# Kernel optimization log

Measured on AMD Instinct MI355X. Metric: run time of the kernel, lower is better.

The kernel has to match this reference:

```python
import jax, jax.numpy as jnp
import numpy as np

DIM = 128

def _mlp2(x, W1, b1, W2, b2):
    return jax.nn.relu(x @ W1 + b1) @ W2 + b2

def setup_inputs() -> dict:
    key = jax.random.key(0)
    ks = jax.random.split(key, 16)
    n_var, n_con, n_nodes = 600000, 400000, 1000000
    s2 = 1.0 / np.sqrt(2.0)
    sd = 1.0 / np.sqrt(DIM)
    inp = {
        'var_node_features': jax.random.normal(ks[0], (n_var, 2), jnp.float32),
        'con_node_features': jax.random.normal(ks[1], (n_con, 2), jnp.float32),
        'node_types': jnp.zeros((n_nodes,), jnp.int32),
        'assoc_var': jnp.arange(n_var, dtype=jnp.int64),
        'assoc_con': jnp.arange(n_con, dtype=jnp.int64),
        # var_mlp params
        'vW1': jax.random.uniform(ks[2], (2, DIM), jnp.float32, -s2, s2),
        'vb1': jnp.zeros((DIM,), jnp.float32),
        'vW2': jax.random.uniform(ks[3], (DIM, DIM), jnp.float32, -sd, sd),
        'vb2': jnp.zeros((DIM,), jnp.float32),
        # con_mlp params
        'cW1': jax.random.uniform(ks[4], (2, DIM), jnp.float32, -s2, s2),
        'cb1': jnp.zeros((DIM,), jnp.float32),
        'cW2': jax.random.uniform(ks[5], (DIM, DIM), jnp.float32, -sd, sd),
        'cb2': jnp.zeros((DIM,), jnp.float32),
        # head params fc1..fc4
        'W1': jax.random.uniform(ks[6], (DIM, DIM), jnp.float32, -sd, sd),
        'b1': jnp.zeros((DIM,), jnp.float32),
        'W2': jax.random.uniform(ks[7], (DIM, DIM), jnp.float32, -sd, sd),
        'b2': jnp.zeros((DIM,), jnp.float32),
        'W3': jax.random.uniform(ks[8], (DIM, DIM), jnp.float32, -sd, sd),
        'b3': jnp.zeros((DIM,), jnp.float32),
        'W4': jax.random.uniform(ks[9], (DIM, 1), jnp.float32, -sd, sd),
        'b4': jnp.zeros((1,), jnp.float32),
    }
    return inp

def reference(var_node_features, con_node_features, node_types, assoc_var, assoc_con,
              vW1, vb1, vW2, vb2, cW1, cb1, cW2, cb2,
              W1, b1, W2, b2, W3, b3, W4, b4):
    n = _mlp2(var_node_features, vW1, vb1, vW2, vb2)   # [n_var, dim]
    e = _mlp2(con_node_features, cW1, cb1, cW2, cb2)   # [n_con, dim]
    # scatter into shared node tensor (var first, then con overwrites)
    x = jnp.zeros((node_types.shape[0], n.shape[-1]), n.dtype)
    x = x.at[assoc_var].set(n)
    x = x.at[assoc_con].set(e)
    # gather variable-node embeddings
    x = x[assoc_var]                                   # [n_var, dim]
    x = jax.nn.relu(x @ W1 + b1)  # dropout is identity in eval mode
    x = jax.nn.relu(x @ W2 + b2)
    x = jax.nn.relu(x @ W3 + b3)
    x = jax.nn.sigmoid(x @ W4 + b4)
    return x.squeeze(-1)
```

## Files before the change

### kernel.cpp

```cpp
#include <hip/hip_runtime.h>
#include <hip/hip_bf16.h>

typedef unsigned short u16;
typedef unsigned int u32;
typedef __attribute__((ext_vector_type(8))) short short8;
typedef __attribute__((ext_vector_type(4))) float f32x4;
typedef __attribute__((ext_vector_type(4))) u32 u32x4;

#define MFMA16(a, b, c) __builtin_amdgcn_mfma_f32_16x16x32_bf16((a), (b), (c), 0, 0, 0)
#define S8(v) __builtin_bit_cast(short8, (v))
#define SBAR() __builtin_amdgcn_sched_barrier(0)

__device__ __forceinline__ u32 pack2(float a, float b) {
    union { __hip_bfloat162 h; u32 u; } v;
    v.h = __float22bfloat162_rn(make_float2(a, b));
    return v.u;
}
__device__ __forceinline__ u16 f2b(float f) {
    union { float f; u32 i; } v; v.f = f;
    u32 x = v.i;
    return (u16)((x + 0x7FFFu + ((x >> 16) & 1u)) >> 16);
}

__device__ __forceinline__ void gl_lds16(const u16* g, u16* l) {
    __builtin_amdgcn_global_load_lds(
        (const __attribute__((address_space(1))) void*)g,
        (__attribute__((address_space(3))) void*)l, 16, 0, 0);
}

__global__ void wt_prep(const float* __restrict__ vW2, const float* __restrict__ cW2,
                        const float* __restrict__ W1f, const float* __restrict__ W2f,
                        const float* __restrict__ W3f, u16* __restrict__ wt) {
    int i = blockIdx.x * 256 + threadIdx.x;
    if (i >= 5 * 16384) return;
    int l = i >> 14, e = i & 16383;
    int fr = e >> 9, lane = (e >> 3) & 63, j = e & 7;
    int ot = fr >> 2, ks = fr & 3;
    int c = lane & 15, q = lane >> 4;
    int f = 32 * ks + 16 * (j >> 2) + 4 * q + (j & 3);
    const float* src = (l == 0) ? vW2 : (l == 1) ? cW2 : (l == 2) ? W1f
                     : (l == 3) ? W2f : W3f;
    wt[i] = f2b(src[f * 128 + ot * 16 + c]);
}


#define STAGE(LSRC, B) do {                                                   \
    _Pragma("unroll")                                                         \
    for (int r = 0; r < 4; ++r) {                                             \
        int ch = r * 8 + wv;                                                  \
        gl_lds16(WT + (size_t)(LSRC) * 16384 + ch * 512 + lane * 8,           \
                 ldsw + (B) * 16384 + ch * 512);                              \
    } } while (0)

#define LDSH(B, QQ, H) do {                                                   \
    const u16* _lp = ldsw + (B) * 16384 + ((QQ) * 8 + (H) * 2) * 512 + lane * 8; \
    wu0 = *(const short8*)(_lp + 0 * 512);                                    \
    wu1 = *(const short8*)(_lp + 1 * 512);                                    \
    wu2 = *(const short8*)(_lp + 4 * 512);                                    \
    wu3 = *(const short8*)(_lp + 5 * 512);                                    \
} while (0)

#define BIVL(LB, QQ) do {                                                     \
    biv0 = *(const f32x4*)(ldsb + (LB) * 128 + ((QQ) * 2 + 0) * 16 + q * 4);  \
    biv1 = *(const f32x4*)(ldsb + (LB) * 128 + ((QQ) * 2 + 1) * 16 + q * 4);  \
} while (0)

#define HALF0(I) do {                                                         \
    ac00 = MFMA16(wu0, S8(I##_r0_k0), biv0);                                  \
    ac01 = MFMA16(wu0, S8(I##_r1_k0), biv0);                                  \
    ac10 = MFMA16(wu2, S8(I##_r0_k0), biv1);                                  \
    ac11 = MFMA16(wu2, S8(I##_r1_k0), biv1);                                  \
    ac00 = MFMA16(wu1, S8(I##_r0_k1), ac00);                                  \
    ac01 = MFMA16(wu1, S8(I##_r1_k1), ac01);                                  \
    ac10 = MFMA16(wu3, S8(I##_r0_k1), ac10);                                  \
    ac11 = MFMA16(wu3, S8(I##_r1_k1), ac11);                                  \
} while (0)

#define HALF1(I) do {                                                         \
    ac00 = MFMA16(wu0, S8(I##_r0_k2), ac00);                                  \
    ac01 = MFMA16(wu0, S8(I##_r1_k2), ac01);                                  \
    ac10 = MFMA16(wu2, S8(I##_r0_k2), ac10);                                  \
    ac11 = MFMA16(wu2, S8(I##_r1_k2), ac11);                                  \
    ac00 = MFMA16(wu1, S8(I##_r0_k3), ac00);                                  \
    ac01 = MFMA16(wu1, S8(I##_r1_k3), ac01);                                  \
    ac10 = MFMA16(wu3, S8(I##_r0_k3), ac10);                                  \
    ac11 = MFMA16(wu3, S8(I##_r1_k3), ac11);                                  \
} while (0)

#define EPI(RELU, ACC, OUT, C0, C1)                                           \
  { float v0 = ACC[0], v1 = ACC[1], v2 = ACC[2], v3 = ACC[3];                 \
    if (RELU) { v0 = fmaxf(v0, 0.f); v1 = fmaxf(v1, 0.f);                     \
                v2 = fmaxf(v2, 0.f); v3 = fmaxf(v3, 0.f); }                   \
    OUT.C0 = pack2(v0, v1); OUT.C1 = pack2(v2, v3); }

#define QUARTER(B, LB, I, O, QQ, RELU) do {                                   \
    BIVL(LB, QQ);                                                             \
    LDSH(B, QQ, 0);                                                           \
    HALF0(I);                                                                 \
    LDSH(B, QQ, 1);                                                           \
    HALF1(I);                                                                 \
    EPI(RELU, ac00, O##_r0_k##QQ, x, y)                                       \
    EPI(RELU, ac01, O##_r1_k##QQ, x, y)                                       \
    EPI(RELU, ac10, O##_r0_k##QQ, z, w)                                       \
    EPI(RELU, ac11, O##_r1_k##QQ, z, w)                                       \
} while (0)

#define LAYER(B, LB, I, O, RELU)                                              \
    QUARTER(B, LB, I, O, 0, RELU);                                            \
    QUARTER(B, LB, I, O, 1, RELU);                                            \
    QUARTER(B, LB, I, O, 2, RELU);                                            \
    QUARTER(B, LB, I, O, 3, RELU);

#define QUARTER_LAST(B, I, QQ) do {                                           \
    BIVL(3, QQ);                                                              \
    f32x4 ww0 = *(const f32x4*)(ldsb + 512 + ((QQ) * 2 + 0) * 16 + q * 4);    \
    f32x4 ww1 = *(const f32x4*)(ldsb + 512 + ((QQ) * 2 + 1) * 16 + q * 4);    \
    LDSH(B, QQ, 0);                                                           \
    HALF0(I);                                                                 \
    LDSH(B, QQ, 1);                                                           \
    HALF1(I);                                                                 \
    pd0 += fmaxf(ac00[0], 0.f) * ww0[0] + fmaxf(ac00[1], 0.f) * ww0[1]        \
         + fmaxf(ac00[2], 0.f) * ww0[2] + fmaxf(ac00[3], 0.f) * ww0[3];       \
    pd0 += fmaxf(ac10[0], 0.f) * ww1[0] + fmaxf(ac10[1], 0.f) * ww1[1]        \
         + fmaxf(ac10[2], 0.f) * ww1[2] + fmaxf(ac10[3], 0.f) * ww1[3];       \
    pd1 += fmaxf(ac01[0], 0.f) * ww0[0] + fmaxf(ac01[1], 0.f) * ww0[1]        \
         + fmaxf(ac01[2], 0.f) * ww0[2] + fmaxf(ac01[3], 0.f) * ww0[3];       \
    pd1 += fmaxf(ac11[0], 0.f) * ww1[0] + fmaxf(ac11[1], 0.f) * ww1[1]        \
         + fmaxf(ac11[2], 0.f) * ww1[2] + fmaxf(ac11[3], 0.f) * ww1[3];       \
} while (0)

#define P0_ROW(V, C0, C1, I0, I1)                                             \
  { float x0 = fmaxf(fmaf(I0, wA.x, fmaf(I1, wB.x, bz.x)), 0.f);              \
    float x1 = fmaxf(fmaf(I0, wA.y, fmaf(I1, wB.y, bz.y)), 0.f);              \
    float x2 = fmaxf(fmaf(I0, wA.z, fmaf(I1, wB.z, bz.z)), 0.f);              \
    float x3 = fmaxf(fmaf(I0, wA.w, fmaf(I1, wB.w, bz.w)), 0.f);              \
    V.C0 = pack2(x0, x1); V.C1 = pack2(x2, x3); }

#define P0_HI(KS, HI, C0, C1)                                                 \
  { const int base = (KS) * 32 + (HI) * 16 + q * 4;                           \
    float4 wA = *(const float4*)(w1p + base);                                 \
    float4 wB = *(const float4*)(w1p + 128 + base);                           \
    float4 bz = *(const float4*)(b1p + base);                                 \
    P0_ROW(a_r0_k##KS, C0, C1, in00, in10)                                    \
    P0_ROW(a_r1_k##KS, C0, C1, in01, in11) }

#define P0_KS(KS) P0_HI(KS, 0, x, y) P0_HI(KS, 1, z, w)

#define P0_IN(RT, I0, I1)                                                     \
  { int g = rowW + (RT) * 16 + c; I0 = 0.f; I1 = 0.f;                         \
    if (g < limit) { float2 t2 = *(const float2*)(fb + 2 * g); I0 = t2.x; I1 = t2.y; } }

__global__ __attribute__((amdgpu_flat_work_group_size(512, 512),
                          amdgpu_waves_per_eu(4))) void
mlp_fused(
    const float* __restrict__ varf, const float* __restrict__ conf,
    const float* __restrict__ vW1, const float* __restrict__ vb1, const float* __restrict__ vb2,
    const float* __restrict__ cW1, const float* __restrict__ cb1, const float* __restrict__ cb2,
    const float* __restrict__ b1,  const float* __restrict__ b2,  const float* __restrict__ b3,
    const float* __restrict__ W4,  const float* __restrict__ b4,
    const u16* __restrict__ WT,   float* __restrict__ out,
    int n_var, int n_con, int nb_con)
{
    const int t = threadIdx.x;
    const int lane = t & 63, wv = t >> 6;
    const int c = lane & 15, q = lane >> 4;
    const int bid = blockIdx.x;
    const bool use_con = (bid < nb_con);
    const int row0 = use_con ? bid * 256 : n_con + (bid - nb_con) * 256;
    const int rowW = row0 + wv * 32;
    const int limit = use_con ? n_con : n_var;

    __shared__ u16 ldsw[2 * 16384];
    __shared__ float ldsb[640];

    u32x4 a_r0_k0, a_r0_k1, a_r0_k2, a_r0_k3;
    u32x4 a_r1_k0, a_r1_k1, a_r1_k2, a_r1_k3;
    u32x4 b_r0_k0, b_r0_k1, b_r0_k2, b_r0_k3;
    u32x4 b_r1_k0, b_r1_k1, b_r1_k2, b_r1_k3;
    short8 wu0, wu1, wu2, wu3;
    f32x4 biv0, biv1;
    f32x4 ac00, ac01, ac10, ac11;

    const float* bs0 = use_con ? cb2 : vb2;

    STAGE((use_con ? 1 : 0), 0);
    STAGE(2, 1);
    {
        int which = t >> 7, idx = t & 127;
        const float* p = (which == 0) ? bs0 : (which == 1) ? b1
                       : (which == 2) ? b2 : b3;
        ldsb[t >= 512 ? 0 : t] = (t >= 512) ? ldsb[0] : p[idx];
        if (t < 128) ldsb[512 + t] = W4[t];
    }
    SBAR();

    {
        const float* w1p = use_con ? cW1 : vW1;
        const float* b1p = use_con ? cb1 : vb1;
        const float* fb  = use_con ? conf : varf;
        float in00, in01, in10, in11;
        P0_IN(0, in00, in10) P0_IN(1, in01, in11)
        P0_KS(0) P0_KS(1) P0_KS(2) P0_KS(3)
    }

    float pd0 = 0.f, pd1 = 0.f;

    __syncthreads();

    LAYER(0, 0, a, b, 0)
    __syncthreads();
    STAGE(3, 0);  SBAR();

    LAYER(1, 1, b, a, 1)
    __syncthreads();
    STAGE(4, 1);  SBAR();

    LAYER(0, 2, a, b, 1)
    __syncthreads();

    QUARTER_LAST(1, b, 0);
    QUARTER_LAST(1, b, 1);
    QUARTER_LAST(1, b, 2);
    QUARTER_LAST(1, b, 3);

    float bias4 = b4[0];
#define REDUCE(PD, RT)                                                        \
    { float v = PD;                                                           \
      v += __shfl_xor(v, 16);                                                 \
      v += __shfl_xor(v, 32);                                                 \
      if (q == 0) {                                                           \
          int g = rowW + (RT) * 16 + c;                                       \
          if (g < limit) out[g] = 1.f / (1.f + __expf(-(v + bias4)));         \
      } }
    REDUCE(pd0, 0) REDUCE(pd1, 1)
#undef REDUCE
}

extern "C" void kernel_launch(void* const* d_in, const int* in_sizes, int n_in,
                              void* d_out, int out_size, void* d_ws, size_t ws_size,
                              hipStream_t stream) {
    const float* varf = (const float*)d_in[0];
    const float* conf = (const float*)d_in[1];
    const float* vW1 = (const float*)d_in[5];
    const float* vb1 = (const float*)d_in[6];
    const float* vW2 = (const float*)d_in[7];
    const float* vb2 = (const float*)d_in[8];
    const float* cW1 = (const float*)d_in[9];
    const float* cb1 = (const float*)d_in[10];
    const float* cW2 = (const float*)d_in[11];
    const float* cb2 = (const float*)d_in[12];
    const float* W1  = (const float*)d_in[13];
    const float* b1  = (const float*)d_in[14];
    const float* W2  = (const float*)d_in[15];
    const float* b2  = (const float*)d_in[16];
    const float* W3  = (const float*)d_in[17];
    const float* b3  = (const float*)d_in[18];
    const float* W4  = (const float*)d_in[19];
    const float* b4  = (const float*)d_in[20];

    int n_var = in_sizes[0] / 2;
    int n_con = in_sizes[1] / 2;
    u16* wt = (u16*)d_ws;

    hipLaunchKernelGGL(wt_prep, dim3(320), dim3(256), 0, stream,
                       vW2, cW2, W1, W2, W3, wt);

    int nb_con = (n_con + 255) / 256;
    int nb_var = (n_var - n_con + 255) / 256;
    hipLaunchKernelGGL(mlp_fused, dim3(nb_con + nb_var), dim3(512), 0, stream,
                       varf, conf, vW1, vb1, vb2, cW1, cb1, cb2,
                       b1, b2, b3, W4, b4, wt, (float*)d_out, n_var, n_con,
                       nb_con);
}
```

Baseline: 177.0 us.

## Switch fused MLP to 32x32x16 MFMA tiles with 64 rows per wave

Replaces the 16x16x32 bf16 MFMA tiling with 32x32x16 MFMAs. The weight pre-layout is reworked to match the new fragment shape, and each of the 4 waves in a 256-thread block now handles 64 rows instead of 32. Weight fragments are double-buffered from LDS across k-steps, and biases and W4 are read directly from global memory instead of a shared bias array. The aim is higher MFMA efficiency and fewer LDS weight reads per FLOP, at the cost of far more activation registers (8 k-slices per row tile) and lower occupancy (2 waves/EU).

```diff
diff --git a/kernel.cpp b/kernel.cpp
--- a/kernel.cpp
+++ b/kernel.cpp
@@ -5,9 +5,10 @@
 typedef unsigned int u32;
 typedef __attribute__((ext_vector_type(8))) short short8;
 typedef __attribute__((ext_vector_type(4))) float f32x4;
+typedef __attribute__((ext_vector_type(16))) float f32x16;
 typedef __attribute__((ext_vector_type(4))) u32 u32x4;
 
-#define MFMA16(a, b, c) __builtin_amdgcn_mfma_f32_16x16x32_bf16((a), (b), (c), 0, 0, 0)
+#define MFMA32(a, b, c) __builtin_amdgcn_mfma_f32_32x32x16_bf16((a), (b), (c), 0, 0, 0)
 #define S8(v) __builtin_bit_cast(short8, (v))
 #define SBAR() __builtin_amdgcn_sched_barrier(0)
 
@@ -27,131 +28,149 @@
         (const __attribute__((address_space(1))) void*)g,
         (__attribute__((address_space(3))) void*)l, 16, 0, 0);
 }
+
 
 __global__ void wt_prep(const float* __restrict__ vW2, const float* __restrict__ cW2,
                         const float* __restrict__ W1f, const float* __restrict__ W2f,
                         const float* __restrict__ W3f, u16* __restrict__ wt) {
     int i = blockIdx.x * 256 + threadIdx.x;
     if (i >= 5 * 16384) return;
-    int l = i >> 14, e = i & 16383;
+    int l5 = i >> 14, e = i & 16383;
     int fr = e >> 9, lane = (e >> 3) & 63, j = e & 7;
-    int ot = fr >> 2, ks = fr & 3;
-    int c = lane & 15, q = lane >> 4;
-    int f = 32 * ks + 16 * (j >> 2) + 4 * q + (j & 3);
-    const float* src = (l == 0) ? vW2 : (l == 1) ? cW2 : (l == 2) ? W1f
-                     : (l == 3) ? W2f : W3f;
-    wt[i] = f2b(src[f * 128 + ot * 16 + c]);
-}
-
+    int ot = fr >> 3, kk = fr & 7;
+    int otp = kk >> 1, s = kk & 1;
+    int m = lane & 31, h = lane >> 5;
+    int inf = otp * 32 + s * 16 + (j & 3) + 8 * (j >> 2) + 4 * h;
+    const float* src = (l5 == 0) ? vW2 : (l5 == 1) ? cW2 : (l5 == 2) ? W1f
+                     : (l5 == 3) ? W2f : W3f;
+    wt[i] = f2b(src[inf * 128 + ot * 32 + m]);
+}
 
 #define STAGE(LSRC, B) do {                                                   \
     _Pragma("unroll")                                                         \
-    for (int r = 0; r < 4; ++r) {                                             \
-        int ch = r * 8 + wv;                                                  \
+    for (int c8 = 0; c8 < 8; ++c8) {                                          \
+        int ch = c8 * 4 + wv;                                                 \
         gl_lds16(WT + (size_t)(LSRC) * 16384 + ch * 512 + lane * 8,           \
                  ldsw + (B) * 16384 + ch * 512);                              \
     } } while (0)
 
-#define LDSH(B, QQ, H) do {                                                   \
-    const u16* _lp = ldsw + (B) * 16384 + ((QQ) * 8 + (H) * 2) * 512 + lane * 8; \
-    wu0 = *(const short8*)(_lp + 0 * 512);                                    \
-    wu1 = *(const short8*)(_lp + 1 * 512);                                    \
-    wu2 = *(const short8*)(_lp + 4 * 512);                                    \
-    wu3 = *(const short8*)(_lp + 5 * 512);                                    \
-} while (0)
-
-#define BIVL(LB, QQ) do {                                                     \
-    biv0 = *(const f32x4*)(ldsb + (LB) * 128 + ((QQ) * 2 + 0) * 16 + q * 4);  \
-    biv1 = *(const f32x4*)(ldsb + (LB) * 128 + ((QQ) * 2 + 1) * 16 + q * 4);  \
-} while (0)
-
-#define HALF0(I) do {                                                         \
-    ac00 = MFMA16(wu0, S8(I##_r0_k0), biv0);                                  \
-    ac01 = MFMA16(wu0, S8(I##_r1_k0), biv0);                                  \
-    ac10 = MFMA16(wu2, S8(I##_r0_k0), biv1);                                  \
-    ac11 = MFMA16(wu2, S8(I##_r1_k0), biv1);                                  \
-    ac00 = MFMA16(wu1, S8(I##_r0_k1), ac00);                                  \
-    ac01 = MFMA16(wu1, S8(I##_r1_k1), ac01);                                  \
-    ac10 = MFMA16(wu3, S8(I##_r0_k1), ac10);                                  \
-    ac11 = MFMA16(wu3, S8(I##_r1_k1), ac11);                                  \
-} while (0)
-
-#define HALF1(I) do {                                                         \
-    ac00 = MFMA16(wu0, S8(I##_r0_k2), ac00);                                  \
-    ac01 = MFMA16(wu0, S8(I##_r1_k2), ac01);                                  \
-    ac10 = MFMA16(wu2, S8(I##_r0_k2), ac10);                                  \
-    ac11 = MFMA16(wu2, S8(I##_r1_k2), ac11);                                  \
-    ac00 = MFMA16(wu1, S8(I##_r0_k3), ac00);                                  \
-    ac01 = MFMA16(wu1, S8(I##_r1_k3), ac01);                                  \
-    ac10 = MFMA16(wu3, S8(I##_r0_k3), ac10);                                  \
-    ac11 = MFMA16(wu3, S8(I##_r1_k3), ac11);                                  \
-} while (0)
-
-#define EPI(RELU, ACC, OUT, C0, C1)                                           \
-  { float v0 = ACC[0], v1 = ACC[1], v2 = ACC[2], v3 = ACC[3];                 \
-    if (RELU) { v0 = fmaxf(v0, 0.f); v1 = fmaxf(v1, 0.f);                     \
-                v2 = fmaxf(v2, 0.f); v3 = fmaxf(v3, 0.f); }                   \
-    OUT.C0 = pack2(v0, v1); OUT.C1 = pack2(v2, v3); }
-
-#define QUARTER(B, LB, I, O, QQ, RELU) do {                                   \
-    BIVL(LB, QQ);                                                             \
-    LDSH(B, QQ, 0);                                                           \
-    HALF0(I);                                                                 \
-    LDSH(B, QQ, 1);                                                           \
-    HALF1(I);                                                                 \
-    EPI(RELU, ac00, O##_r0_k##QQ, x, y)                                       \
-    EPI(RELU, ac01, O##_r1_k##QQ, x, y)                                       \
-    EPI(RELU, ac10, O##_r0_k##QQ, z, w)                                       \
-    EPI(RELU, ac11, O##_r1_k##QQ, z, w)                                       \
-} while (0)
-
-#define LAYER(B, LB, I, O, RELU)                                              \
-    QUARTER(B, LB, I, O, 0, RELU);                                            \
-    QUARTER(B, LB, I, O, 1, RELU);                                            \
-    QUARTER(B, LB, I, O, 2, RELU);                                            \
-    QUARTER(B, LB, I, O, 3, RELU);
-
-#define QUARTER_LAST(B, I, QQ) do {                                           \
-    BIVL(3, QQ);                                                              \
-    f32x4 ww0 = *(const f32x4*)(ldsb + 512 + ((QQ) * 2 + 0) * 16 + q * 4);    \
-    f32x4 ww1 = *(const f32x4*)(ldsb + 512 + ((QQ) * 2 + 1) * 16 + q * 4);    \
-    LDSH(B, QQ, 0);                                                           \
-    HALF0(I);                                                                 \
-    LDSH(B, QQ, 1);                                                           \
-    HALF1(I);                                                                 \
-    pd0 += fmaxf(ac00[0], 0.f) * ww0[0] + fmaxf(ac00[1], 0.f) * ww0[1]        \
-         + fmaxf(ac00[2], 0.f) * ww0[2] + fmaxf(ac00[3], 0.f) * ww0[3];       \
-    pd0 += fmaxf(ac10[0], 0.f) * ww1[0] + fmaxf(ac10[1], 0.f) * ww1[1]        \
-         + fmaxf(ac10[2], 0.f) * ww1[2] + fmaxf(ac10[3], 0.f) * ww1[3];       \
-    pd1 += fmaxf(ac01[0], 0.f) * ww0[0] + fmaxf(ac01[1], 0.f) * ww0[1]        \
-         + fmaxf(ac01[2], 0.f) * ww0[2] + fmaxf(ac01[3], 0.f) * ww0[3];       \
-    pd1 += fmaxf(ac11[0], 0.f) * ww1[0] + fmaxf(ac11[1], 0.f) * ww1[1]        \
-         + fmaxf(ac11[2], 0.f) * ww1[2] + fmaxf(ac11[3], 0.f) * ww1[3];       \
-} while (0)
-
-#define P0_ROW(V, C0, C1, I0, I1)                                             \
-  { float x0 = fmaxf(fmaf(I0, wA.x, fmaf(I1, wB.x, bz.x)), 0.f);              \
-    float x1 = fmaxf(fmaf(I0, wA.y, fmaf(I1, wB.y, bz.y)), 0.f);              \
-    float x2 = fmaxf(fmaf(I0, wA.z, fmaf(I1, wB.z, bz.z)), 0.f);              \
-    float x3 = fmaxf(fmaf(I0, wA.w, fmaf(I1, wB.w, bz.w)), 0.f);              \
-    V.C0 = pack2(x0, x1); V.C1 = pack2(x2, x3); }
-
-#define P0_HI(KS, HI, C0, C1)                                                 \
-  { const int base = (KS) * 32 + (HI) * 16 + q * 4;                           \
-    float4 wA = *(const float4*)(w1p + base);                                 \
-    float4 wB = *(const float4*)(w1p + 128 + base);                           \
-    float4 bz = *(const float4*)(b1p + base);                                 \
-    P0_ROW(a_r0_k##KS, C0, C1, in00, in10)                                    \
-    P0_ROW(a_r1_k##KS, C0, C1, in01, in11) }
-
-#define P0_KS(KS) P0_HI(KS, 0, x, y) P0_HI(KS, 1, z, w)
-
-#define P0_IN(RT, I0, I1)                                                     \
-  { int g = rowW + (RT) * 16 + c; I0 = 0.f; I1 = 0.f;                         \
-    if (g < limit) { float2 t2 = *(const float2*)(fb + 2 * g); I0 = t2.x; I1 = t2.y; } }
-
-__global__ __attribute__((amdgpu_flat_work_group_size(512, 512),
-                          amdgpu_waves_per_eu(4))) void
+#define LDW2(BASE, OT0, OT1, KK, S) do {                                      \
+    w##S##0 = *(const short8*)((BASE) + ((OT0) * 8 + (KK)) * 512 + lane * 8); \
+    w##S##1 = *(const short8*)((BASE) + ((OT1) * 8 + (KK)) * 512 + lane * 8); \
+} while (0)
+
+#define BIN(BSRC, OT, V) do {                                                 \
+    f32x4 _t0 = *(const f32x4*)((BSRC) + (OT) * 32 + 4 * h);                  \
+    f32x4 _t1 = *(const f32x4*)((BSRC) + (OT) * 32 + 4 * h + 8);              \
+    f32x4 _t2 = *(const f32x4*)((BSRC) + (OT) * 32 + 4 * h + 16);             \
+    f32x4 _t3 = *(const f32x4*)((BSRC) + (OT) * 32 + 4 * h + 24);             \
+    V = (f32x16){_t0.x, _t0.y, _t0.z, _t0.w, _t1.x, _t1.y, _t1.z, _t1.w,      \
+                 _t2.x, _t2.y, _t2.z, _t2.w, _t3.x, _t3.y, _t3.z, _t3.w};     \
+} while (0)
+
+#define KSTEP0(S, I)                                                          \
+    ac00 = MFMA32(w##S##0, S8(I##_r0_k0), bin0);                              \
+    ac01 = MFMA32(w##S##0, S8(I##_r1_k0), bin0);                              \
+    ac10 = MFMA32(w##S##1, S8(I##_r0_k0), bin1);                              \
+    ac11 = MFMA32(w##S##1, S8(I##_r1_k0), bin1);
+
+#define KSTEP(S, I, KK)                                                       \
+    ac00 = MFMA32(w##S##0, S8(I##_r0_k##KK), ac00);                           \
+    ac01 = MFMA32(w##S##0, S8(I##_r1_k##KK), ac01);                           \
+    ac10 = MFMA32(w##S##1, S8(I##_r0_k##KK), ac10);                           \
+    ac11 = MFMA32(w##S##1, S8(I##_r1_k##KK), ac11);
+
+#define EPIT(RELU, ACC, O0, O1) do {                                          \
+    float e0 = ACC[0], e1 = ACC[1], e2 = ACC[2], e3 = ACC[3];                 \
+    float e4 = ACC[4], e5 = ACC[5], e6 = ACC[6], e7 = ACC[7];                 \
+    float e8 = ACC[8], e9 = ACC[9], e10 = ACC[10], e11 = ACC[11];             \
+    float e12 = ACC[12], e13 = ACC[13], e14 = ACC[14], e15 = ACC[15];         \
+    if (RELU) {                                                               \
+        e0 = fmaxf(e0, 0.f); e1 = fmaxf(e1, 0.f); e2 = fmaxf(e2, 0.f);        \
+        e3 = fmaxf(e3, 0.f); e4 = fmaxf(e4, 0.f); e5 = fmaxf(e5, 0.f);        \
+        e6 = fmaxf(e6, 0.f); e7 = fmaxf(e7, 0.f); e8 = fmaxf(e8, 0.f);        \
+        e9 = fmaxf(e9, 0.f); e10 = fmaxf(e10, 0.f); e11 = fmaxf(e11, 0.f);    \
+        e12 = fmaxf(e12, 0.f); e13 = fmaxf(e13, 0.f); e14 = fmaxf(e14, 0.f);  \
+        e15 = fmaxf(e15, 0.f);                                                \
+    }                                                                         \
+    O0.x = pack2(e0, e1);  O0.y = pack2(e2, e3);                              \
+    O0.z = pack2(e4, e5);  O0.w = pack2(e6, e7);                              \
+    O1.x = pack2(e8, e9);  O1.y = pack2(e10, e11);                            \
+    O1.z = pack2(e12, e13); O1.w = pack2(e14, e15);                           \
+} while (0)
+
+#define EPIP(O, KA, KB, KC, KD, RELU)                                         \
+    EPIT(RELU, ac00, O##_r0_k##KA, O##_r0_k##KB);                             \
+    EPIT(RELU, ac01, O##_r1_k##KA, O##_r1_k##KB);                             \
+    EPIT(RELU, ac10, O##_r0_k##KC, O##_r0_k##KD);                             \
+    EPIT(RELU, ac11, O##_r1_k##KC, O##_r1_k##KD);
+
+#define LASTT(ACC, W16, PD)                                                   \
+    PD += fmaxf(ACC[0], 0.f) * W16[0]  + fmaxf(ACC[1], 0.f) * W16[1]          \
+        + fmaxf(ACC[2], 0.f) * W16[2]  + fmaxf(ACC[3], 0.f) * W16[3]          \
+        + fmaxf(ACC[4], 0.f) * W16[4]  + fmaxf(ACC[5], 0.f) * W16[5]          \
+        + fmaxf(ACC[6], 0.f) * W16[6]  + fmaxf(ACC[7], 0.f) * W16[7]          \
+        + fmaxf(ACC[8], 0.f) * W16[8]  + fmaxf(ACC[9], 0.f) * W16[9]          \
+        + fmaxf(ACC[10], 0.f) * W16[10] + fmaxf(ACC[11], 0.f) * W16[11]       \
+        + fmaxf(ACC[12], 0.f) * W16[12] + fmaxf(ACC[13], 0.f) * W16[13]       \
+        + fmaxf(ACC[14], 0.f) * W16[14] + fmaxf(ACC[15], 0.f) * W16[15];
+
+#define PASS(BASE, BS, I, O, OT0, OT1, KA, KB, KC, KD, RELU)                  \
+    LDW2(BASE, OT0, OT1, 0, u); SBAR();                                       \
+    LDW2(BASE, OT0, OT1, 1, v); SBAR();                                       \
+    BIN(BS, OT0, bin0); BIN(BS, OT1, bin1);                                   \
+    KSTEP0(u, I)                                                              \
+    LDW2(BASE, OT0, OT1, 2, u); SBAR(); KSTEP(v, I, 1)                        \
+    LDW2(BASE, OT0, OT1, 3, v); SBAR(); KSTEP(u, I, 2)                        \
+    LDW2(BASE, OT0, OT1, 4, u); SBAR(); KSTEP(v, I, 3)                        \
+    LDW2(BASE, OT0, OT1, 5, v); SBAR(); KSTEP(u, I, 4)                        \
+    LDW2(BASE, OT0, OT1, 6, u); SBAR(); KSTEP(v, I, 5)                        \
+    LDW2(BASE, OT0, OT1, 7, v); SBAR(); KSTEP(u, I, 6)                        \
+    KSTEP(v, I, 7)                                                            \
+    EPIP(O, KA, KB, KC, KD, RELU)
+
+#define LASTP(BASE, BS, I, OT0, OT1)                                          \
+    LDW2(BASE, OT0, OT1, 0, u); SBAR();                                       \
+    LDW2(BASE, OT0, OT1, 1, v); SBAR();                                       \
+    BIN(BS, OT0, bin0); BIN(BS, OT1, bin1);                                   \
+    KSTEP0(u, I)                                                              \
+    LDW2(BASE, OT0, OT1, 2, u); SBAR(); KSTEP(v, I, 1)                        \
+    LDW2(BASE, OT0, OT1, 3, v); SBAR(); KSTEP(u, I, 2)                        \
+    LDW2(BASE, OT0, OT1, 4, u); SBAR(); KSTEP(v, I, 3)                        \
+    LDW2(BASE, OT0, OT1, 5, v); SBAR(); KSTEP(u, I, 4)                        \
+    LDW2(BASE, OT0, OT1, 6, u); SBAR(); KSTEP(v, I, 5)                        \
+    LDW2(BASE, OT0, OT1, 7, v); SBAR(); KSTEP(u, I, 6)                        \
+    KSTEP(v, I, 7)                                                            \
+    BIN(W4, OT0, bin0); BIN(W4, OT1, bin1);                                   \
+    LASTT(ac00, bin0, pd0) LASTT(ac01, bin0, pd1)                             \
+    LASTT(ac10, bin1, pd0) LASTT(ac11, bin1, pd1)
+
+#define P0F(V, I0, I1)                                                        \
+  { float x0 = fmaxf(fmaf(I0, wA0.x, fmaf(I1, wB0.x, bz0.x)), 0.f);           \
+    float x1 = fmaxf(fmaf(I0, wA0.y, fmaf(I1, wB0.y, bz0.y)), 0.f);           \
+    float x2 = fmaxf(fmaf(I0, wA0.z, fmaf(I1, wB0.z, bz0.z)), 0.f);           \
+    float x3 = fmaxf(fmaf(I0, wA0.w, fmaf(I1, wB0.w, bz0.w)), 0.f);           \
+    float y0 = fmaxf(fmaf(I0, wA1.x, fmaf(I1, wB1.x, bz1.x)), 0.f);           \
+    float y1 = fmaxf(fmaf(I0, wA1.y, fmaf(I1, wB1.y, bz1.y)), 0.f);           \
+    float y2 = fmaxf(fmaf(I0, wA1.z, fmaf(I1, wB1.z, bz1.z)), 0.f);           \
+    float y3 = fmaxf(fmaf(I0, wA1.w, fmaf(I1, wB1.w, bz1.w)), 0.f);           \
+    V.x = pack2(x0, x1); V.y = pack2(x2, x3);                                 \
+    V.z = pack2(y0, y1); V.w = pack2(y2, y3); }
+
+#define P0K(KK) do {                                                          \
+    const int bf = ((KK) >> 1) * 32 + ((KK) & 1) * 16 + 4 * h;                \
+    float4 wA0 = *(const float4*)(w1p + bf);                                  \
+    float4 wA1 = *(const float4*)(w1p + bf + 8);                              \
+    float4 wB0 = *(const float4*)(w1p + 128 + bf);                            \
+    float4 wB1 = *(const float4*)(w1p + 128 + bf + 8);                        \
+    float4 bz0 = *(const float4*)(b1p + bf);                                  \
+    float4 bz1 = *(const float4*)(b1p + bf + 8);                              \
+    P0F(a_r0_k##KK, in00, in10)                                               \
+    P0F(a_r1_k##KK, in01, in11)                                               \
+} while (0)
+
+__global__ __attribute__((amdgpu_flat_work_group_size(256, 256),
+                          amdgpu_waves_per_eu(2, 2))) void
 mlp_fused(
     const float* __restrict__ varf, const float* __restrict__ conf,
     const float* __restrict__ vW1, const float* __restrict__ vb1, const float* __restrict__ vb2,
@@ -163,77 +182,79 @@
 {
     const int t = threadIdx.x;
     const int lane = t & 63, wv = t >> 6;
-    const int c = lane & 15, q = lane >> 4;
+    const int cl = lane & 31, h = lane >> 5;
     const int bid = blockIdx.x;
     const bool use_con = (bid < nb_con);
     const int row0 = use_con ? bid * 256 : n_con + (bid - nb_con) * 256;
-    const int rowW = row0 + wv * 32;
+    const int rowW = row0 + wv * 64;
     const int limit = use_con ? n_con : n_var;
 
     __shared__ u16 ldsw[2 * 16384];
-    __shared__ float ldsb[640];
-
-    u32x4 a_r0_k0, a_r0_k1, a_r0_k2, a_r0_k3;
-    u32x4 a_r1_k0, a_r1_k1, a_r1_k2, a_r1_k3;
-    u32x4 b_r0_k0, b_r0_k1, b_r0_k2, b_r0_k3;
-    u32x4 b_r1_k0, b_r1_k1, b_r1_k2, b_r1_k3;
-    short8 wu0, wu1, wu2, wu3;
-    f32x4 biv0, biv1;
-    f32x4 ac00, ac01, ac10, ac11;
+
+    u32x4 a_r0_k0, a_r0_k1, a_r0_k2, a_r0_k3, a_r0_k4, a_r0_k5, a_r0_k6, a_r0_k7;
+    u32x4 a_r1_k0, a_r1_k1, a_r1_k2, a_r1_k3, a_r1_k4, a_r1_k5, a_r1_k6, a_r1_k7;
+    u32x4 b_r0_k0, b_r0_k1, b_r0_k2, b_r0_k3, b_r0_k4, b_r0_k5, b_r0_k6, b_r0_k7;
+    u32x4 b_r1_k0, b_r1_k1, b_r1_k2, b_r1_k3, b_r1_k4, b_r1_k5, b_r1_k6, b_r1_k7;
+    short8 wu0, wu1, wv0, wv1;
+    f32x16 bin0, bin1;
+    f32x16 ac00, ac01, ac10, ac11;
 
     const float* bs0 = use_con ? cb2 : vb2;
+    const float* w1p = use_con ? cW1 : vW1;
+    const float* b1p = use_con ? cb1 : vb1;
+    const float* fb  = use_con ? conf : varf;
+
+    float in00 = 0.f, in10 = 0.f, in01 = 0.f, in11 = 0.f;
+    {
+        int g0 = rowW + cl, g1 = rowW + 32 + cl;
+        if (g0 < limit) { float2 t2 = *(const float2*)(fb + 2 * g0); in00 = t2.x; in10 = t2.y; }
+        if (g1 < limit) { float2 t2 = *(const float2*)(fb + 2 * g1); in01 = t2.x; in11 = t2.y; }
+    }
 
     STAGE((use_con ? 1 : 0), 0);
     STAGE(2, 1);
+    SBAR();
+
+    P0K(0); P0K(1); P0K(2); P0K(3); P0K(4); P0K(5); P0K(6); P0K(7);
+
+    float pd0 = 0.f, pd1 = 0.f;
+
+    __syncthreads();
+
+    PASS(ldsw,         bs0, a, b, 0, 1, 0, 1, 2, 3, 0)
+    PASS(ldsw,         bs0, a, b, 2, 3, 4, 5, 6, 7, 0)
+    __syncthreads();
+    STAGE(3, 0);  SBAR();
+
+    PASS(ldsw + 16384, b1, b, a, 0, 1, 0, 1, 2, 3, 1)
+    PASS(ldsw + 16384, b1, b, a, 2, 3, 4, 5, 6, 7, 1)
+    __syncthreads();
+    STAGE(4, 1);  SBAR();
+
+    PASS(ldsw,         b2, a, b, 0, 1, 0, 1, 2, 3, 1)
+    PASS(ldsw,         b2, a, b, 2, 3, 4, 5, 6, 7, 1)
+    __syncthreads();
+
+    LASTP(ldsw + 16384, b3, b, 0, 1)
+    LASTP(ldsw + 16384, b3, b, 2, 3)
+
+    float bias4 = b4[0];
     {
-        int which = t >> 7, idx = t & 127;
-        const float* p = (which == 0) ? bs0 : (which == 1) ? b1
-                       : (which == 2) ? b2 : b3;
-        ldsb[t >= 512 ? 0 : t] = (t >= 512) ? ldsb[0] : p[idx];
-        if (t < 128) ldsb[512 + t] = W4[t];
+        float v = pd0;
+        v += __shfl_xor(v, 32);
+        if (h == 0) {
+            int g = rowW + cl;
+            if (g < limit) out[g] = 1.f / (1.f + __expf(-(v + bias4)));
+        }
     }
-    SBAR();
-
     {
-        const float* w1p = use_con ? cW1 : vW1;
-        const float* b1p = use_con ? cb1 : vb1;
-        const float* fb  = use_con ? conf : varf;
-        float in00, in01, in10, in11;
-        P0_IN(0, in00, in10) P0_IN(1, in01, in11)
-        P0_KS(0) P0_KS(1) P0_KS(2) P0_KS(3)
+        float v = pd1;
+        v += __shfl_xor(v, 32);
+        if (h == 0) {
+            int g = rowW + 32 + cl;
+            if (g < limit) out[g] = 1.f / (1.f + __expf(-(v + bias4)));
+        }
     }
-
-    float pd0 = 0.f, pd1 = 0.f;
-
-    __syncthreads();
-
-    LAYER(0, 0, a, b, 0)
-    __syncthreads();
-    STAGE(3, 0);  SBAR();
-
-    LAYER(1, 1, b, a, 1)
-    __syncthreads();
-    STAGE(4, 1);  SBAR();
-
-    LAYER(0, 2, a, b, 1)
-    __syncthreads();
-
-    QUARTER_LAST(1, b, 0);
-    QUARTER_LAST(1, b, 1);
-    QUARTER_LAST(1, b, 2);
-    QUARTER_LAST(1, b, 3);
-
-    float bias4 = b4[0];
-#define REDUCE(PD, RT)                                                        \
-    { float v = PD;                                                           \
-      v += __shfl_xor(v, 16);                                                 \
-      v += __shfl_xor(v, 32);                                                 \
-      if (q == 0) {                                                           \
-          int g = rowW + (RT) * 16 + c;                                       \
-          if (g < limit) out[g] = 1.f / (1.f + __expf(-(v + bias4)));         \
-      } }
-    REDUCE(pd0, 0) REDUCE(pd1, 1)
-#undef REDUCE
 }
 
 extern "C" void kernel_launch(void* const* d_in, const int* in_sizes, int n_in,
@@ -267,7 +288,7 @@
 
     int nb_con = (n_con + 255) / 256;
     int nb_var = (n_var - n_con + 255) / 256;
-    hipLaunchKernelGGL(mlp_fused, dim3(nb_con + nb_var), dim3(512), 0, stream,
+    hipLaunchKernelGGL(mlp_fused, dim3(nb_con + nb_var), dim3(256), 0, stream,
                        varf, conf, vW1, vb1, vb2, cW1, cb1, cb2,
                        b1, b2, b3, W4, b4, wt, (float*)d_out, n_var, n_con,
                        nb_con);
```

New measurement: 185.6 us. 4.9% more time.
